# Kernel tuning notes

Hardware: AMD Instinct MI355X
Metric: run time of the kernel (lower is better)

The kernel has to match this reference:

```python
import jax, jax.numpy as jnp
import numpy as np

H = 16          # num query heads
G = 4           # num kv heads (groups)
MAX_POS = 128   # max relative position


def setup_inputs() -> dict:
    key = jax.random.key(0)
    ks = jax.random.split(key, 6)
    B, T, D = 8, 1024, 1024
    hd = D // H
    s = 0.02
    return {
        "x": jax.random.normal(ks[0], (B, T, D), jnp.float32),
        "Wq": jax.random.normal(ks[1], (D, D), jnp.float32) * s,
        "Wk": jax.random.normal(ks[2], (hd * G, D), jnp.float32) * s,
        "Wv": jax.random.normal(ks[3], (hd * G, D), jnp.float32) * s,
        "Wo": jax.random.normal(ks[4], (D, D), jnp.float32) * s,
        "E": jax.random.normal(ks[5], (2 * MAX_POS - 1, hd), jnp.float32) * s,
    }


def reference(x, Wq, Wk, Wv, Wo, E):
    B, T, D = x.shape
    hd = D // H
    r = H // G  # kv repeat factor

    # projections (torch nn.Linear convention: y = x @ W.T)
    q = (x @ Wq.T).reshape(B, T, H, hd).transpose(0, 2, 1, 3)  # [B,H,T,hd]
    k = (x @ Wk.T).reshape(B, T, G, hd)                         # [B,T,G,hd]
    v = (x @ Wv.T).reshape(B, T, G, hd)

    # GQA: query head h uses kv group h // r  (matches repeat_interleave)
    k = jnp.repeat(k, r, axis=2).transpose(0, 2, 1, 3)  # [B,H,T,hd]
    v = jnp.repeat(v, r, axis=2).transpose(0, 2, 1, 3)  # [B,H,T,hd]

    q = q * (1.0 / hd) ** 0.5
    scores = jnp.einsum("bhqd,bhkd->bhqk", q, k)  # [B,H,T,T]

    # relative position bias: R[i,j] = E[clamp(j - i) + MAX_POS - 1]
    pos = jnp.arange(T)
    dist = jnp.clip(pos[None, :] - pos[:, None], -MAX_POS + 1, MAX_POS - 1) + MAX_POS - 1
    R = E[dist]  # [T,T,hd]
    # original einsum 'bhd,thd->bht' with q=[B*H, Tq, hd], R=[Tk, Tq, hd]:
    # bias[b,h,q,kpos] = sum_d q[b,h,q,d] * R[kpos, q, d]
    bias = jnp.einsum("bhqd,kqd->bhqk", q, R)
    scores = scores + bias

    attn = jax.nn.softmax(scores, axis=-1)
    out = jnp.einsum("bhqk,bhkd->bhqd", attn, v)         # [B,H,T,hd]
    out = out.transpose(0, 2, 1, 3).reshape(B, T, D)      # [B,T,D]
    return out @ Wo.T
```

## Files before the change

### kernel.cpp

```cpp
#include <hip/hip_runtime.h>
#include <hip/hip_bf16.h>
#include <cstdint>
#include <cstddef>

typedef __hip_bfloat16 bf16;
typedef __attribute__((ext_vector_type(8))) __bf16 bf16x8;
typedef __attribute__((ext_vector_type(4))) float floatx4;

#define GPTR(p) ((const __attribute__((address_space(1))) void*)(p))
#define LPTR(p) ((__attribute__((address_space(3))) void*)(p))

__device__ __forceinline__ floatx4 mfma16(bf16x8 a, bf16x8 b, floatx4 c) {
  return __builtin_amdgcn_mfma_f32_16x16x32_bf16(a, b, c, 0, 0, 0);
}

__global__ __launch_bounds__(256) void cvt_bf16(const float* __restrict__ in,
                                                bf16* __restrict__ out, int n4) {
  for (int i = blockIdx.x * 256 + threadIdx.x; i < n4; i += gridDim.x * 256) {
    float4 v = ((const float4*)in)[i];
    alignas(8) bf16 t[4] = {__float2bfloat16(v.x), __float2bfloat16(v.y),
                            __float2bfloat16(v.z), __float2bfloat16(v.w)};
    *(uint64_t*)(out + (size_t)i * 4) = *(const uint64_t*)t;
  }
}

__global__ __launch_bounds__(256) void gemm_qkv(
    const bf16* __restrict__ A, const bf16* __restrict__ Wq,
    const bf16* __restrict__ Wk, const bf16* __restrict__ Wv,
    bf16* __restrict__ qout, bf16* __restrict__ kout,
    bf16* __restrict__ vTout) {
  __shared__ alignas(16) bf16 As[128 * 32];
  __shared__ alignas(16) bf16 Bs[128 * 32];
  const int tid = threadIdx.x;
  const int lane = tid & 63;
  const int w = tid >> 6;
  const int wr = w >> 1, wc = w & 1;
  const int quad = lane >> 4, c = lane & 15;
  const int m0 = blockIdx.y * 128;
  const int nb = blockIdx.x;

  int mode, nloc;
  const bf16* Wp;
  if (nb < 8) {
    mode = 1; Wp = Wq + (size_t)nb * 128 * 1024; nloc = nb * 128;
  } else if (nb < 10) {
    mode = 2; Wp = Wk + (size_t)(nb - 8) * 128 * 1024; nloc = (nb - 8) * 128;
  } else {
    mode = 3; Wp = Wv + (size_t)(nb - 10) * 128 * 1024; nloc = (nb - 10) * 128;
  }

  const int i0 = tid, i1 = tid + 256;
  const bf16* ga0 = A + (size_t)(m0 + (i0 >> 2)) * 1024 + (i0 & 3) * 8;
  const bf16* ga1 = A + (size_t)(m0 + (i1 >> 2)) * 1024 + (i1 & 3) * 8;
  const bf16* gb0 = Wp + (size_t)(i0 >> 2) * 1024 + (i0 & 3) * 8;
  const bf16* gb1 = Wp + (size_t)(i1 >> 2) * 1024 + (i1 & 3) * 8;

  floatx4 acc[4][4] = {};

  for (int kt = 0; kt < 32; ++kt) {
    if (kt) __syncthreads();
    __builtin_amdgcn_global_load_lds(GPTR(ga0), LPTR(&As[i0 * 8]), 16, 0, 0);
    __builtin_amdgcn_global_load_lds(GPTR(ga1), LPTR(&As[i1 * 8]), 16, 0, 0);
    __builtin_amdgcn_global_load_lds(GPTR(gb0), LPTR(&Bs[i0 * 8]), 16, 0, 0);
    __builtin_amdgcn_global_load_lds(GPTR(gb1), LPTR(&Bs[i1 * 8]), 16, 0, 0);
    ga0 += 32; ga1 += 32; gb0 += 32; gb1 += 32;
    __syncthreads();
    bf16x8 af[4], bfr[4];
#pragma unroll
    for (int i = 0; i < 4; ++i)
      af[i] = *(const bf16x8*)&As[(wr * 64 + i * 16 + c) * 32 + quad * 8];
#pragma unroll
    for (int j = 0; j < 4; ++j)
      bfr[j] = *(const bf16x8*)&Bs[(wc * 64 + j * 16 + c) * 32 + quad * 8];
#pragma unroll
    for (int i = 0; i < 4; ++i)
#pragma unroll
      for (int j = 0; j < 4; ++j)
        acc[i][j] = mfma16(af[i], bfr[j], acc[i][j]);
  }

  if (mode == 3) {
#pragma unroll
    for (int i = 0; i < 4; ++i)
#pragma unroll
      for (int j = 0; j < 4; ++j) {
        int m = m0 + wr * 64 + i * 16 + quad * 4;
        int n = nloc + wc * 64 + j * 16 + c;
        int b = m >> 10, t = m & 1023, g = n >> 6, d = n & 63;
        alignas(8) bf16 tmp[4];
#pragma unroll
        for (int r = 0; r < 4; ++r) tmp[r] = __float2bfloat16(acc[i][j][r]);
        *(uint64_t*)(vTout + (((size_t)(b * 4 + g)) * 64 + d) * 1024 + t) =
            *(const uint64_t*)tmp;
      }
    return;
  }

  const float scale = (mode == 1) ? 0.125f : 1.0f;
#pragma unroll
  for (int i = 0; i < 4; ++i)
#pragma unroll
    for (int j = 0; j < 4; ++j)
#pragma unroll
      for (int r = 0; r < 4; ++r) {
        int m = m0 + wr * 64 + i * 16 + quad * 4 + r;
        int n = nloc + wc * 64 + j * 16 + c;
        int b = m >> 10, t = m & 1023;
        bf16 v = __float2bfloat16(acc[i][j][r] * scale);
        if (mode == 1) {
          int h = n >> 6;
          qout[(((size_t)(b * 16 + h)) * 1024 + t) * 64 + (n & 63)] = v;
        } else {
          int g = n >> 6;
          kout[(((size_t)(b * 4 + g)) * 1024 + t) * 64 + (n & 63)] = v;
        }
      }
}

__global__ __launch_bounds__(256) void gemm_o(const bf16* __restrict__ A,
                                              const bf16* __restrict__ W,
                                              float* __restrict__ out) {
  __shared__ alignas(16) bf16 As[128 * 32];
  __shared__ alignas(16) bf16 Bs[128 * 32];
  const int tid = threadIdx.x;
  const int lane = tid & 63;
  const int w = tid >> 6;
  const int wr = w >> 1, wc = w & 1;
  const int quad = lane >> 4, c = lane & 15;
  const int m0 = blockIdx.y * 128, n0 = blockIdx.x * 128;

  const int i0 = tid, i1 = tid + 256;
  const bf16* ga0 = A + (size_t)(m0 + (i0 >> 2)) * 1024 + (i0 & 3) * 8;
  const bf16* ga1 = A + (size_t)(m0 + (i1 >> 2)) * 1024 + (i1 & 3) * 8;
  const bf16* gb0 = W + (size_t)(n0 + (i0 >> 2)) * 1024 + (i0 & 3) * 8;
  const bf16* gb1 = W + (size_t)(n0 + (i1 >> 2)) * 1024 + (i1 & 3) * 8;

  floatx4 acc[4][4] = {};

  for (int kt = 0; kt < 32; ++kt) {
    if (kt) __syncthreads();
    __builtin_amdgcn_global_load_lds(GPTR(ga0), LPTR(&As[i0 * 8]), 16, 0, 0);
    __builtin_amdgcn_global_load_lds(GPTR(ga1), LPTR(&As[i1 * 8]), 16, 0, 0);
    __builtin_amdgcn_global_load_lds(GPTR(gb0), LPTR(&Bs[i0 * 8]), 16, 0, 0);
    __builtin_amdgcn_global_load_lds(GPTR(gb1), LPTR(&Bs[i1 * 8]), 16, 0, 0);
    ga0 += 32; ga1 += 32; gb0 += 32; gb1 += 32;
    __syncthreads();
    bf16x8 af[4], bfr[4];
#pragma unroll
    for (int i = 0; i < 4; ++i)
      af[i] = *(const bf16x8*)&As[(wr * 64 + i * 16 + c) * 32 + quad * 8];
#pragma unroll
    for (int j = 0; j < 4; ++j)
      bfr[j] = *(const bf16x8*)&Bs[(wc * 64 + j * 16 + c) * 32 + quad * 8];
#pragma unroll
    for (int i = 0; i < 4; ++i)
#pragma unroll
      for (int j = 0; j < 4; ++j)
        acc[i][j] = mfma16(af[i], bfr[j], acc[i][j]);
  }

#pragma unroll
  for (int i = 0; i < 4; ++i)
#pragma unroll
    for (int j = 0; j < 4; ++j)
#pragma unroll
      for (int r = 0; r < 4; ++r) {
        int m = m0 + wr * 64 + i * 16 + quad * 4 + r;
        int n = n0 + wc * 64 + j * 16 + c;
        out[(size_t)m * 1024 + n] = acc[i][j][r];
      }
}

__device__ __forceinline__ void stage_tile_swz(const bf16* __restrict__ g,
                                               int gstride, bf16* __restrict__ dst,
                                               int tid) {
#pragma unroll
  for (int s = 0; s < 2; ++s) {
    int f = s * 256 + tid;
    int r = f >> 3, cb = f & 7;
    int cbg = cb ^ (r & 7);
    __builtin_amdgcn_global_load_lds(GPTR(g + (size_t)r * gstride + cbg * 8),
                                     LPTR(dst + f * 8), 16, 0, 0);
  }
}

__device__ __forceinline__ bf16x8 read_frag_swz(const bf16* __restrict__ tile,
                                                int row, int cb) {
  return *(const bf16x8*)&tile[row * 64 + ((cb ^ (row & 7)) * 8)];
}

__device__ __forceinline__ void attn_tile(
    int t0, const bf16* __restrict__ kbase, const bf16* __restrict__ vbase,
    bf16* __restrict__ curK, bf16* __restrict__ nxtK,
    bf16* __restrict__ curV, bf16* __restrict__ nxtV,
    const bf16* __restrict__ rowE, int qb, int tid, int w, int quad, int c,
    bf16x8 qf0, bf16x8 qf1, float blo, float bhi, float& mrow, float& lrow,
    floatx4 (&o)[4]) {
  const int nt0 = (t0 + 64) & 1023;
  stage_tile_swz(vbase + nt0, 1024, nxtV, tid);
  stage_tile_swz(kbase + (size_t)nt0 * 64, 64, nxtK, tid);
  floatx4 S[4];
#pragma unroll
  for (int j = 0; j < 4; ++j) {
    bf16x8 kf0 = read_frag_swz(curK, j * 16 + c, quad);
    bf16x8 kf1 = read_frag_swz(curK, j * 16 + c, quad + 4);
    floatx4 z = {};
    z = mfma16(kf0, qf0, z);
    S[j] = mfma16(kf1, qf1, z);
  }
  const int dlt0 = qb + c - t0;
  if (t0 <= qb - 190) {
#pragma unroll
    for (int j = 0; j < 4; ++j)
#pragma unroll
      for (int r = 0; r < 4; ++r) S[j][r] += blo;
  } else if (t0 >= qb + 142) {
#pragma unroll
    for (int j = 0; j < 4; ++j)
#pragma unroll
      for (int r = 0; r < 4; ++r) S[j][r] += bhi;
  } else {
#pragma unroll
    for (int j = 0; j < 4; ++j)
#pragma unroll
      for (int r = 0; r < 4; ++r) {
        int dlt = dlt0 - j * 16 - quad * 4 - r;
        dlt = dlt > 127 ? 127 : (dlt < -127 ? -127 : dlt);
        S[j][r] += __bfloat162float(rowE[dlt + 127]);
      }
  }
  float mx = -1e30f;
#pragma unroll
  for (int j = 0; j < 4; ++j)
#pragma unroll
    for (int r = 0; r < 4; ++r) mx = fmaxf(mx, S[j][r]);
  mx = fmaxf(mx, __shfl_xor(mx, 16, 64));
  mx = fmaxf(mx, __shfl_xor(mx, 32, 64));
  float nm = fmaxf(mrow, mx);
  float alpha = __expf(mrow - nm);
  float rs = 0.f;
#pragma unroll
  for (int j = 0; j < 4; ++j)
#pragma unroll
    for (int r = 0; r < 4; ++r) {
      float p = __expf(S[j][r] - nm);
      S[j][r] = p;
      rs += p;
    }
  rs += __shfl_xor(rs, 16, 64);
  rs += __shfl_xor(rs, 32, 64);
  lrow = lrow * alpha + rs;
  mrow = nm;
  __builtin_amdgcn_sched_barrier(0);
  __builtin_amdgcn_s_barrier();
  __builtin_amdgcn_sched_barrier(0);
  bf16* rowP = curK + (size_t)(w * 16 + c) * 72;
#pragma unroll
  for (int j = 0; j < 4; ++j) {
    alignas(8) bf16 tmp[4];
#pragma unroll
    for (int r = 0; r < 4; ++r) tmp[r] = __float2bfloat16(S[j][r]);
    *(uint64_t*)(rowP + j * 16 + quad * 4) = *(const uint64_t*)tmp;
  }
  float av[4];
#pragma unroll
  for (int r = 0; r < 4; ++r) av[r] = __shfl(alpha, quad * 4 + r, 64);
#pragma unroll
  for (int jj = 0; jj < 4; ++jj)
#pragma unroll
    for (int r = 0; r < 4; ++r) o[jj][r] *= av[r];
  __threadfence_block();
  __builtin_amdgcn_wave_barrier();
  bf16x8 pf0 = *(const bf16x8*)(rowP + quad * 8);
  bf16x8 pf1 = *(const bf16x8*)(rowP + 32 + quad * 8);
#pragma unroll
  for (int jj = 0; jj < 4; ++jj) {
    bf16x8 vf0 = read_frag_swz(curV, jj * 16 + c, quad);
    bf16x8 vf1 = read_frag_swz(curV, jj * 16 + c, quad + 4);
    o[jj] = mfma16(pf0, vf0, o[jj]);
    o[jj] = mfma16(pf1, vf1, o[jj]);
  }
  asm volatile("s_waitcnt vmcnt(0)" ::: "memory");
  __builtin_amdgcn_sched_barrier(0);
  __builtin_amdgcn_s_barrier();
  __builtin_amdgcn_sched_barrier(0);
}

__global__ __launch_bounds__(256, 2) void attn_kernel(
    const bf16* __restrict__ q_ws, const bf16* __restrict__ k_ws,
    const bf16* __restrict__ vT, const float* __restrict__ E,
    bf16* __restrict__ out) {
  __shared__ alignas(16) bf16 qEl[64 * 264];
  __shared__ alignas(16) bf16 Ka[64 * 72];
  __shared__ alignas(16) bf16 Kc[64 * 72];
  __shared__ alignas(16) bf16 Va[64 * 64];
  __shared__ alignas(16) bf16 Vc[64 * 64];
  const int tid = threadIdx.x;
  const int lane = tid & 63, w = tid >> 6;
  const int quad = lane >> 4, c = lane & 15;
  const int bh = blockIdx.y;
  const int b = bh >> 4, h = bh & 15, g = h >> 2;
  const int qb = blockIdx.x * 64 + w * 16;

  const bf16* kbase = k_ws + (size_t)(b * 4 + g) * 1024 * 64;
  const bf16* vbase = vT + (size_t)(b * 4 + g) * 64 * 1024;

  stage_tile_swz(kbase, 64, Ka, tid);
  stage_tile_swz(vbase, 1024, Va, tid);

  const bf16* qrow = q_ws + ((size_t)bh * 1024 + qb + c) * 64;
  bf16x8 qf0 = *(const bf16x8*)(qrow + quad * 8);
  bf16x8 qf1 = *(const bf16x8*)(qrow + 32 + quad * 8);

  for (int jn = 0; jn < 16; ++jn) {
    int er = jn * 16 + c;
    er = er > 254 ? 254 : er;
    const float* Ep = E + (size_t)er * 64;
    float4 e0 = *(const float4*)(Ep + quad * 8);
    float4 e1 = *(const float4*)(Ep + quad * 8 + 4);
    float4 e2 = *(const float4*)(Ep + 32 + quad * 8);
    float4 e3 = *(const float4*)(Ep + 32 + quad * 8 + 4);
    alignas(16) bf16 t0b[8] = {
        __float2bfloat16(e0.x), __float2bfloat16(e0.y), __float2bfloat16(e0.z),
        __float2bfloat16(e0.w), __float2bfloat16(e1.x), __float2bfloat16(e1.y),
        __float2bfloat16(e1.z), __float2bfloat16(e1.w)};
    alignas(16) bf16 t1b[8] = {
        __float2bfloat16(e2.x), __float2bfloat16(e2.y), __float2bfloat16(e2.z),
        __float2bfloat16(e2.w), __float2bfloat16(e3.x), __float2bfloat16(e3.y),
        __float2bfloat16(e3.z), __float2bfloat16(e3.w)};
    floatx4 a = {};
    a = mfma16(qf0, *(const bf16x8*)t0b, a);
    a = mfma16(qf1, *(const bf16x8*)t1b, a);
#pragma unroll
    for (int r = 0; r < 4; ++r)
      qEl[(w * 16 + quad * 4 + r) * 264 + jn * 16 + c] = __float2bfloat16(a[r]);
  }
  __syncthreads();

  const bf16* rowE = qEl + (size_t)(w * 16 + c) * 264;
  float mrow = -1e30f, lrow = 0.f;
  floatx4 o[4] = {};
  const float blo = __bfloat162float(rowE[254]);
  const float bhi = __bfloat162float(rowE[0]);

#pragma unroll 1
  for (int tp = 0; tp < 8; ++tp) {
    attn_tile(tp * 128, kbase, vbase, Ka, Kc, Va, Vc, rowE, qb, tid, w, quad,
              c, qf0, qf1, blo, bhi, mrow, lrow, o);
    attn_tile(tp * 128 + 64, kbase, vbase, Kc, Ka, Vc, Va, rowE, qb, tid, w,
              quad, c, qf0, qf1, blo, bhi, mrow, lrow, o);
  }

  float lr4[4];
#pragma unroll
  for (int r = 0; r < 4; ++r) lr4[r] = __shfl(lrow, quad * 4 + r, 64);
#pragma unroll
  for (int jj = 0; jj < 4; ++jj)
#pragma unroll
    for (int r = 0; r < 4; ++r) {
      int qi = qb + quad * 4 + r;
      out[(((size_t)b * 1024 + qi) * 16 + h) * 64 + jj * 16 + c] =
          __float2bfloat16(o[jj][r] / lr4[r]);
    }
}

extern "C" void kernel_launch(void* const* d_in, const int* in_sizes, int n_in,
                              void* d_out, int out_size, void* d_ws,
                              size_t ws_size, hipStream_t stream) {
  const float* x = (const float*)d_in[0];
  const float* Wq = (const float*)d_in[1];
  const float* Wk = (const float*)d_in[2];
  const float* Wv = (const float*)d_in[3];
  const float* Wo = (const float*)d_in[4];
  const float* E = (const float*)d_in[5];

  char* ws = (char*)d_ws;
  bf16* q_ws = (bf16*)d_out;
  bf16* x_bf = (bf16*)((char*)d_out + (16ull << 20));
  bf16* k_ws = (bf16*)(ws);
  bf16* vT = (bf16*)(ws + (4ull << 20));
  bf16* attn = (bf16*)(ws + (8ull << 20));
  bf16* Wq_bf = (bf16*)(ws + (8ull << 20));
  bf16* Wk_bf = (bf16*)(ws + (10ull << 20));
  bf16* Wv_bf = (bf16*)(ws + (10ull << 20) + (512ull << 10));
  bf16* Wo_bf = (bf16*)(ws);
  float* outp = (float*)d_out;

  cvt_bf16<<<2048, 256, 0, stream>>>(x, x_bf, 2097152);
  cvt_bf16<<<1024, 256, 0, stream>>>(Wq, Wq_bf, 262144);
  cvt_bf16<<<256, 256, 0, stream>>>(Wk, Wk_bf, 65536);
  cvt_bf16<<<256, 256, 0, stream>>>(Wv, Wv_bf, 65536);
  gemm_qkv<<<dim3(12, 64), 256, 0, stream>>>(x_bf, Wq_bf, Wk_bf, Wv_bf,
                                             q_ws, k_ws, vT);
  attn_kernel<<<dim3(16, 128), 256, 0, stream>>>(q_ws, k_ws, vT, E, attn);
  cvt_bf16<<<1024, 256, 0, stream>>>(Wo, Wo_bf, 262144);
  gemm_o<<<dim3(8, 64), 256, 0, stream>>>(attn, Wo_bf, outp);
}
```

Baseline: 293.9 us.

## Load V fragments directly to registers, add lazy softmax rescale and priorities

V tiles are no longer staged through LDS. Each lane loads its V fragments straight from global memory into registers, which frees the Va/Vc shared buffers, and the occupancy hint rises from 2 to 3 blocks per CU. The online softmax now rescales only when some row max grows by more than 8, and the row-sum reduction across lanes is deferred to the end. MFMA sections are wrapped in s_setprio. The cost is exposed global-load latency per tile and more register pressure under the tighter launch bound.

```diff
diff --git a/kernel.cpp b/kernel.cpp
--- a/kernel.cpp
+++ b/kernel.cpp
@@ -12,6 +12,15 @@
 
 __device__ __forceinline__ floatx4 mfma16(bf16x8 a, bf16x8 b, floatx4 c) {
   return __builtin_amdgcn_mfma_f32_16x16x32_bf16(a, b, c, 0, 0, 0);
+}
+
+__device__ __forceinline__ bf16x8 gload16(const bf16* p) {
+  bf16x8 r;
+  asm volatile("global_load_dwordx4 %0, %1, off"
+               : "=v"(r)
+               : "v"(p)
+               : "memory");
+  return r;
 }
 
 __global__ __launch_bounds__(256) void cvt_bf16(const float* __restrict__ in,
@@ -192,14 +201,20 @@
 __device__ __forceinline__ void attn_tile(
     int t0, const bf16* __restrict__ kbase, const bf16* __restrict__ vbase,
     bf16* __restrict__ curK, bf16* __restrict__ nxtK,
-    bf16* __restrict__ curV, bf16* __restrict__ nxtV,
     const bf16* __restrict__ rowE, int qb, int tid, int w, int quad, int c,
-    bf16x8 qf0, bf16x8 qf1, float blo, float bhi, float& mrow, float& lrow,
+    bf16x8 qf0, bf16x8 qf1, float blo, float bhi, float& mrow, float& lpart,
     floatx4 (&o)[4]) {
+  bf16x8 vf[4][2];
+#pragma unroll
+  for (int jj = 0; jj < 4; ++jj) {
+    const bf16* vr = vbase + (size_t)(jj * 16 + c) * 1024 + t0 + quad * 8;
+    vf[jj][0] = gload16(vr);
+    vf[jj][1] = gload16(vr + 32);
+  }
   const int nt0 = (t0 + 64) & 1023;
-  stage_tile_swz(vbase + nt0, 1024, nxtV, tid);
   stage_tile_swz(kbase + (size_t)nt0 * 64, 64, nxtK, tid);
   floatx4 S[4];
+  __builtin_amdgcn_s_setprio(1);
 #pragma unroll
   for (int j = 0; j < 4; ++j) {
     bf16x8 kf0 = read_frag_swz(curK, j * 16 + c, quad);
@@ -208,6 +223,7 @@
     z = mfma16(kf0, qf0, z);
     S[j] = mfma16(kf1, qf1, z);
   }
+  __builtin_amdgcn_s_setprio(0);
   const int dlt0 = qb + c - t0;
   if (t0 <= qb - 190) {
 #pragma unroll
@@ -229,28 +245,36 @@
         S[j][r] += __bfloat162float(rowE[dlt + 127]);
       }
   }
-  float mx = -1e30f;
+  float mx = S[0][0];
 #pragma unroll
   for (int j = 0; j < 4; ++j)
 #pragma unroll
     for (int r = 0; r < 4; ++r) mx = fmaxf(mx, S[j][r]);
-  mx = fmaxf(mx, __shfl_xor(mx, 16, 64));
-  mx = fmaxf(mx, __shfl_xor(mx, 32, 64));
-  float nm = fmaxf(mrow, mx);
-  float alpha = __expf(mrow - nm);
+  if (__ballot(mx > mrow + 8.f)) {
+    float fm = fmaxf(mx, __shfl_xor(mx, 16, 64));
+    fm = fmaxf(fm, __shfl_xor(fm, 32, 64));
+    float nm = fmaxf(mrow, fm);
+    float alpha = __expf(mrow - nm);
+    float av[4];
+#pragma unroll
+    for (int r = 0; r < 4; ++r) av[r] = __shfl(alpha, quad * 4 + r, 64);
+#pragma unroll
+    for (int jj = 0; jj < 4; ++jj)
+#pragma unroll
+      for (int r = 0; r < 4; ++r) o[jj][r] *= av[r];
+    lpart *= alpha;
+    mrow = nm;
+  }
   float rs = 0.f;
 #pragma unroll
   for (int j = 0; j < 4; ++j)
 #pragma unroll
     for (int r = 0; r < 4; ++r) {
-      float p = __expf(S[j][r] - nm);
+      float p = __expf(S[j][r] - mrow);
       S[j][r] = p;
       rs += p;
     }
-  rs += __shfl_xor(rs, 16, 64);
-  rs += __shfl_xor(rs, 32, 64);
-  lrow = lrow * alpha + rs;
-  mrow = nm;
+  lpart += rs;
   __builtin_amdgcn_sched_barrier(0);
   __builtin_amdgcn_s_barrier();
   __builtin_amdgcn_sched_barrier(0);
@@ -262,39 +286,32 @@
     for (int r = 0; r < 4; ++r) tmp[r] = __float2bfloat16(S[j][r]);
     *(uint64_t*)(rowP + j * 16 + quad * 4) = *(const uint64_t*)tmp;
   }
-  float av[4];
-#pragma unroll
-  for (int r = 0; r < 4; ++r) av[r] = __shfl(alpha, quad * 4 + r, 64);
-#pragma unroll
-  for (int jj = 0; jj < 4; ++jj)
-#pragma unroll
-    for (int r = 0; r < 4; ++r) o[jj][r] *= av[r];
   __threadfence_block();
   __builtin_amdgcn_wave_barrier();
   bf16x8 pf0 = *(const bf16x8*)(rowP + quad * 8);
   bf16x8 pf1 = *(const bf16x8*)(rowP + 32 + quad * 8);
+  asm volatile("s_waitcnt vmcnt(2)" ::: "memory");
+  __builtin_amdgcn_sched_barrier(0);
+  __builtin_amdgcn_s_setprio(1);
 #pragma unroll
   for (int jj = 0; jj < 4; ++jj) {
-    bf16x8 vf0 = read_frag_swz(curV, jj * 16 + c, quad);
-    bf16x8 vf1 = read_frag_swz(curV, jj * 16 + c, quad + 4);
-    o[jj] = mfma16(pf0, vf0, o[jj]);
-    o[jj] = mfma16(pf1, vf1, o[jj]);
-  }
+    o[jj] = mfma16(pf0, vf[jj][0], o[jj]);
+    o[jj] = mfma16(pf1, vf[jj][1], o[jj]);
+  }
+  __builtin_amdgcn_s_setprio(0);
   asm volatile("s_waitcnt vmcnt(0)" ::: "memory");
   __builtin_amdgcn_sched_barrier(0);
   __builtin_amdgcn_s_barrier();
   __builtin_amdgcn_sched_barrier(0);
 }
 
-__global__ __launch_bounds__(256, 2) void attn_kernel(
+__global__ __launch_bounds__(256, 3) void attn_kernel(
     const bf16* __restrict__ q_ws, const bf16* __restrict__ k_ws,
     const bf16* __restrict__ vT, const float* __restrict__ E,
     bf16* __restrict__ out) {
   __shared__ alignas(16) bf16 qEl[64 * 264];
   __shared__ alignas(16) bf16 Ka[64 * 72];
   __shared__ alignas(16) bf16 Kc[64 * 72];
-  __shared__ alignas(16) bf16 Va[64 * 64];
-  __shared__ alignas(16) bf16 Vc[64 * 64];
   const int tid = threadIdx.x;
   const int lane = tid & 63, w = tid >> 6;
   const int quad = lane >> 4, c = lane & 15;
@@ -306,7 +323,6 @@
   const bf16* vbase = vT + (size_t)(b * 4 + g) * 64 * 1024;
 
   stage_tile_swz(kbase, 64, Ka, tid);
-  stage_tile_swz(vbase, 1024, Va, tid);
 
   const bf16* qrow = q_ws + ((size_t)bh * 1024 + qb + c) * 64;
   bf16x8 qf0 = *(const bf16x8*)(qrow + quad * 8);
@@ -338,22 +354,24 @@
   __syncthreads();
 
   const bf16* rowE = qEl + (size_t)(w * 16 + c) * 264;
-  float mrow = -1e30f, lrow = 0.f;
+  float mrow = -1e30f, lpart = 0.f;
   floatx4 o[4] = {};
   const float blo = __bfloat162float(rowE[254]);
   const float bhi = __bfloat162float(rowE[0]);
 
 #pragma unroll 1
   for (int tp = 0; tp < 8; ++tp) {
-    attn_tile(tp * 128, kbase, vbase, Ka, Kc, Va, Vc, rowE, qb, tid, w, quad,
-              c, qf0, qf1, blo, bhi, mrow, lrow, o);
-    attn_tile(tp * 128 + 64, kbase, vbase, Kc, Ka, Vc, Va, rowE, qb, tid, w,
-              quad, c, qf0, qf1, blo, bhi, mrow, lrow, o);
-  }
-
+    attn_tile(tp * 128, kbase, vbase, Ka, Kc, rowE, qb, tid, w, quad, c,
+              qf0, qf1, blo, bhi, mrow, lpart, o);
+    attn_tile(tp * 128 + 64, kbase, vbase, Kc, Ka, rowE, qb, tid, w, quad, c,
+              qf0, qf1, blo, bhi, mrow, lpart, o);
+  }
+
+  float lsum = lpart + __shfl_xor(lpart, 16, 64);
+  lsum += __shfl_xor(lsum, 32, 64);
   float lr4[4];
 #pragma unroll
-  for (int r = 0; r < 4; ++r) lr4[r] = __shfl(lrow, quad * 4 + r, 64);
+  for (int r = 0; r < 4; ++r) lr4[r] = __shfl(lsum, quad * 4 + r, 64);
 #pragma unroll
   for (int jj = 0; jj < 4; ++jj)
 #pragma unroll
```

Measured after the change: 345.3 us. +17.5%, slower.
